# Kernel tuning notes

Hardware: AMD Instinct MI355X
Metric: run time of the kernel (lower is better)

## Reference

```python
import jax, jax.numpy as jnp
import numpy as np

B, A, C, H, W = 16, 5, 512, 16, 16


def _affine_grid(theta, Hh, Ww):
    # torch F.affine_grid, align_corners=False (default). theta: [2,3]
    xs = (2.0 * jnp.arange(Ww, dtype=jnp.float32) + 1.0) / Ww - 1.0  # [W]
    ys = (2.0 * jnp.arange(Hh, dtype=jnp.float32) + 1.0) / Hh - 1.0  # [H]
    gx = theta[0, 0] * xs[None, :] + theta[0, 1] * ys[:, None] + theta[0, 2]  # [H,W]
    gy = theta[1, 0] * xs[None, :] + theta[1, 1] * ys[:, None] + theta[1, 2]  # [H,W]
    return gx, gy


def _grid_sample(img, gx, gy):
    # torch F.grid_sample, bilinear, padding_mode='zeros', align_corners=False
    # img: [C,H,W]; gx,gy: [H,W] normalized coords
    C_, Hh, Ww = img.shape
    ix = ((gx + 1.0) * Ww - 1.0) * 0.5
    iy = ((gy + 1.0) * Hh - 1.0) * 0.5
    x0 = jnp.floor(ix); y0 = jnp.floor(iy)
    x1 = x0 + 1.0;      y1 = y0 + 1.0
    wx1 = ix - x0; wx0 = 1.0 - wx1
    wy1 = iy - y0; wy0 = 1.0 - wy1

    def gather(xi, yi):
        inb = (xi >= 0) & (xi < Ww) & (yi >= 0) & (yi < Hh)
        xc = jnp.clip(xi, 0, Ww - 1).astype(jnp.int32)
        yc = jnp.clip(yi, 0, Hh - 1).astype(jnp.int32)
        return img[:, yc, xc] * inb[None].astype(img.dtype)  # [C,H,W]

    return (gather(x0, y0) * (wx0 * wy0)[None] + gather(x1, y0) * (wx1 * wy0)[None]
          + gather(x0, y1) * (wx0 * wy1)[None] + gather(x1, y1) * (wx1 * wy1)[None])


def _warp(nb_feat, nb_warp):
    # nb_feat: [C,H,W] neighbor feature; nb_warp: [4,4] pose matrix
    zero = jnp.zeros((), dtype=jnp.float32)
    one = jnp.ones((), dtype=jnp.float32)
    theta_rot = jnp.stack([
        jnp.stack([nb_warp[0, 0], nb_warp[0, 1], zero]),
        jnp.stack([nb_warp[1, 0], nb_warp[1, 1], zero])])  # [2,3]
    gx_r, gy_r = _affine_grid(theta_rot, H, W)
    feat_rot = _grid_sample(nb_feat, gx_r, gy_r)
    x_trans = 4.0 * nb_warp[0, 3] / 128.0
    y_trans = -(4.0 * nb_warp[1, 3]) / 128.0
    theta_trans = jnp.stack([
        jnp.stack([one, zero, x_trans]),
        jnp.stack([zero, one, y_trans])])
    gx_t, gy_t = _affine_grid(theta_trans, H, W)
    return _grid_sample(feat_rot, gx_t, gy_t)  # [C,H,W]


def _fuse_one(local_b, trans_b, n):
    # local_b: [A,C,H,W], trans_b: [A,A,4,4], n: scalar num_agent
    # pair[i,j] = warp of agent j's feature into agent i's frame
    pair = jax.vmap(lambda t_i: jax.vmap(_warp)(local_b, t_i))(trans_b)  # [A,A,C,H,W]
    idx = jnp.arange(A)
    mask = (idx[:, None] != idx[None, :]) & (idx[:, None] < n) & (idx[None, :] < n)
    return local_b + jnp.einsum('ij,ijchw->ichw', mask.astype(local_b.dtype), pair)


def setup_inputs() -> dict:
    key = jax.random.key(0)
    k1, k2, k3, k4 = jax.random.split(key, 4)
    feat_maps = jax.random.normal(k1, (A * B, C, H, W), dtype=jnp.float32)
    # realistic near-rigid pose matrices: rotation block + translation column
    ang = jax.random.uniform(k2, (B, A, A), minval=-0.5, maxval=0.5)
    tr = jax.random.normal(k3, (B, A, A, 2), dtype=jnp.float32) * 8.0
    tm = jnp.zeros((B, A, A, 4, 4), dtype=jnp.float32)
    tm = tm.at[..., 0, 0].set(jnp.cos(ang)).at[..., 0, 1].set(-jnp.sin(ang))
    tm = tm.at[..., 1, 0].set(jnp.sin(ang)).at[..., 1, 1].set(jnp.cos(ang))
    tm = tm.at[..., 0, 3].set(tr[..., 0]).at[..., 1, 3].set(tr[..., 1])
    tm = tm.at[..., 2, 2].set(1.0).at[..., 3, 3].set(1.0)
    num_agent = jax.random.randint(k4, (B, A), 1, 6, dtype=jnp.int64) if jax.config.jax_enable_x64 else jax.random.randint(k4, (B, A), 1, 6, dtype=jnp.int32)
    return {"feat_maps": feat_maps, "trans_matrices": tm, "num_agent_tensor": num_agent}


def reference(feat_maps, trans_matrices, num_agent_tensor):
    # feat_maps is agent-major blocks of size B (feat_maps[B*i:B*(i+1)] is agent i)
    local = feat_maps.reshape(A, B, C, H, W).transpose(1, 0, 2, 3, 4)  # [B,A,C,H,W]
    fused = jax.vmap(_fuse_one)(local, trans_matrices, num_agent_tensor[:, 0])
    # agents2batch: concat agents along batch dim -> [A*B,C,H,W]
    return fused.transpose(1, 0, 2, 3, 4).reshape(A * B, C, H, W)
```

## Files before the change

kernel.cpp:

```cpp
#include <hip/hip_runtime.h>

#define NB 16
#define NA 5
#define NC 512
#define HW 256

typedef float f4 __attribute__((ext_vector_type(4)));

__global__ __launch_bounds__(256) void fafmimo_fuse_kernel(
    const float* __restrict__ feat,
    const float* __restrict__ trans,
    const int*   __restrict__ numa,
    float*       __restrict__ out)
{
    __shared__ f4 lds_src[NA][HW];
    __shared__ f4 lds_fr[HW];

    const int bx = blockIdx.x;
    const int b  = bx & (NB - 1);
    const int g  = bx >> 4;
    const int c0 = g << 2;
    const int p  = threadIdx.x;
    const int x  = p & 15, y = p >> 4;
    const float fx = (float)x - 7.5f;
    const float fy = (float)y - 7.5f;
    const int n = numa[b * NA];

    f4 local_v[NA];
#pragma unroll
    for (int a = 0; a < NA; ++a) {
        const float* src = feat + ((a * NB + b) * NC + c0) * HW + p;
        f4 v;
        v.x = src[0];
        v.y = src[HW];
        v.z = src[2 * HW];
        v.w = src[3 * HW];
        lds_src[a][p] = v;
        local_v[a] = v;
    }
    __syncthreads();

    for (int i = 0; i < NA; ++i) {
        f4 acc = local_v[i];

        if (i < n) {
            for (int j = 0; j < n; ++j) {
                if (j == i) continue;

                const f4* twv = (const f4*)(trans + (((b * NA) + i) * NA + j) * 16);
                const f4 row0 = twv[0];
                const f4 row1 = twv[1];

                const float ixr = row0.x * fx + row0.y * fy + 7.5f;
                const float iyr = row1.x * fx + row1.y * fy + 7.5f;
                const float fx0 = floorf(ixr), fy0 = floorf(iyr);
                const float wx1 = ixr - fx0, wx0 = 1.0f - wx1;
                const float wy1 = iyr - fy0, wy0 = 1.0f - wy1;
                const int ix0 = (int)fx0, iy0 = (int)fy0;
                const int ix1 = ix0 + 1,  iy1 = iy0 + 1;
                const float mx0 = (ix0 >= 0 && ix0 < 16) ? wx0 : 0.0f;
                const float mx1 = (ix1 >= 0 && ix1 < 16) ? wx1 : 0.0f;
                const float my0 = (iy0 >= 0 && iy0 < 16) ? wy0 : 0.0f;
                const float my1 = (iy1 >= 0 && iy1 < 16) ? wy1 : 0.0f;
                const int cx0 = min(max(ix0, 0), 15), cx1 = min(max(ix1, 0), 15);
                const int cy0 = min(max(iy0, 0), 15), cy1 = min(max(iy1, 0), 15);
                const f4 v00 = lds_src[j][cy0 * 16 + cx0];
                const f4 v01 = lds_src[j][cy0 * 16 + cx1];
                const f4 v10 = lds_src[j][cy1 * 16 + cx0];
                const f4 v11 = lds_src[j][cy1 * 16 + cx1];
                const f4 fr = (v00 * mx0 + v01 * mx1) * my0
                            + (v10 * mx0 + v11 * mx1) * my1;

                __syncthreads();
                lds_fr[p] = fr;
                __syncthreads();

                const float dx = 0.25f * row0.w;
                const float dy = -0.25f * row1.w;
                const float fdx = floorf(dx), fdy = floorf(dy);
                const float tx1 = dx - fdx, tx0 = 1.0f - tx1;
                const float ty1 = dy - fdy, ty0 = 1.0f - ty1;
                const int ox = x + (int)fdx;
                const int oy = y + (int)fdy;
                const float wxa = (ox     >= 0 && ox     < 16) ? tx0 : 0.0f;
                const float wxb = (ox + 1 >= 0 && ox + 1 < 16) ? tx1 : 0.0f;
                const float wya = (oy     >= 0 && oy     < 16) ? ty0 : 0.0f;
                const float wyb = (oy + 1 >= 0 && oy + 1 < 16) ? ty1 : 0.0f;
                const int cxa = min(max(ox, 0), 15),     cxb = min(max(ox + 1, 0), 15);
                const int cya = min(max(oy, 0), 15),     cyb = min(max(oy + 1, 0), 15);
                const f4 t00 = lds_fr[cya * 16 + cxa];
                const f4 t01 = lds_fr[cya * 16 + cxb];
                const f4 t10 = lds_fr[cyb * 16 + cxa];
                const f4 t11 = lds_fr[cyb * 16 + cxb];
                acc += (t00 * wxa + t01 * wxb) * wya
                     + (t10 * wxa + t11 * wxb) * wyb;
            }
        }

        float* dst = out + ((i * NB + b) * NC + c0) * HW + p;
        dst[0]      = acc.x;
        dst[HW]     = acc.y;
        dst[2 * HW] = acc.z;
        dst[3 * HW] = acc.w;
    }
}

extern "C" void kernel_launch(void* const* d_in, const int* in_sizes, int n_in,
                              void* d_out, int out_size, void* d_ws, size_t ws_size,
                              hipStream_t stream) {
    const float* feat  = (const float*)d_in[0];
    const float* trans = (const float*)d_in[1];
    const int*   numa  = (const int*)d_in[2];
    float* out = (float*)d_out;

    fafmimo_fuse_kernel<<<dim3(NB * (NC / 4)), dim3(256), 0, stream>>>(
        feat, trans, numa, out);
}
```

Before: 115.8 us.

## Store features as fp16 in LDS, fuse two-stage warp without syncs

Features are stored in LDS as packed fp16 with 8 channels per thread instead of 4 fp32, which halves the block count and doubles per-block channel work. The two-stage rotate-then-translate sampling is merged: each output pixel directly evaluates the four rotated samples its translation bilinear tap needs. That removes the intermediate LDS buffer and the two __syncthreads per neighbour. The cost is four times more rotation-sample work per neighbour, plus fp16 rounding of the inputs and of the interpolation arithmetic. That rounding may break accuracy tolerance, and the local feature is also rounded through fp16.

```diff
diff --git a/kernel.cpp b/kernel.cpp
--- a/kernel.cpp
+++ b/kernel.cpp
@@ -6,6 +6,33 @@
 #define HW 256
 
 typedef float f4 __attribute__((ext_vector_type(4)));
+typedef _Float16 h8 __attribute__((ext_vector_type(8)));
+
+static __device__ __forceinline__ h8 splat8(_Float16 v) {
+    h8 r = {v, v, v, v, v, v, v, v};
+    return r;
+}
+
+static __device__ __forceinline__ h8 rot_sample(const h8* __restrict__ src,
+                                                float ixr, float iyr, float ws) {
+    const float fx0 = floorf(ixr), fy0 = floorf(iyr);
+    const float wx1 = ixr - fx0,   wy1 = iyr - fy0;
+    const int ix0 = (int)fx0, iy0 = (int)fy0;
+    const int ix1 = ix0 + 1,  iy1 = iy0 + 1;
+    const float mx0 = (ix0 >= 0 && ix0 < 16) ? (1.0f - wx1) : 0.0f;
+    const float mx1 = (ix1 >= 0 && ix1 < 16) ? wx1 : 0.0f;
+    const float my0 = (iy0 >= 0 && iy0 < 16) ? (1.0f - wy1) * ws : 0.0f;
+    const float my1 = (iy1 >= 0 && iy1 < 16) ? wy1 * ws : 0.0f;
+    const int cx0 = min(max(ix0, 0), 15), cx1 = min(max(ix1, 0), 15);
+    const int cy0 = min(max(iy0, 0), 15), cy1 = min(max(iy1, 0), 15);
+    const h8 v00 = src[cy0 * 16 + cx0];
+    const h8 v01 = src[cy0 * 16 + cx1];
+    const h8 v10 = src[cy1 * 16 + cx0];
+    const h8 v11 = src[cy1 * 16 + cx1];
+    const h8 hx0 = splat8((_Float16)mx0), hx1 = splat8((_Float16)mx1);
+    const h8 hy0 = splat8((_Float16)my0), hy1 = splat8((_Float16)my1);
+    return (v00 * hx0 + v01 * hx1) * hy0 + (v10 * hx0 + v11 * hx1) * hy1;
+}
 
 __global__ __launch_bounds__(256) void fafmimo_fuse_kernel(
     const float* __restrict__ feat,
@@ -13,67 +40,41 @@
     const int*   __restrict__ numa,
     float*       __restrict__ out)
 {
-    __shared__ f4 lds_src[NA][HW];
-    __shared__ f4 lds_fr[HW];
+    __shared__ h8 lds_src[NA][HW];
 
     const int bx = blockIdx.x;
     const int b  = bx & (NB - 1);
     const int g  = bx >> 4;
-    const int c0 = g << 2;
+    const int c0 = g << 3;
     const int p  = threadIdx.x;
     const int x  = p & 15, y = p >> 4;
-    const float fx = (float)x - 7.5f;
-    const float fy = (float)y - 7.5f;
-    const int n = numa[b * NA];
+    const int n  = numa[b * NA];
 
-    f4 local_v[NA];
 #pragma unroll
     for (int a = 0; a < NA; ++a) {
         const float* src = feat + ((a * NB + b) * NC + c0) * HW + p;
-        f4 v;
-        v.x = src[0];
-        v.y = src[HW];
-        v.z = src[2 * HW];
-        v.w = src[3 * HW];
+        h8 v;
+#pragma unroll
+        for (int k = 0; k < 8; ++k) v[k] = (_Float16)src[k * HW];
         lds_src[a][p] = v;
-        local_v[a] = v;
     }
     __syncthreads();
 
     for (int i = 0; i < NA; ++i) {
-        f4 acc = local_v[i];
+        const h8 lv = lds_src[i][p];
+        float acc[8];
+#pragma unroll
+        for (int k = 0; k < 8; ++k) acc[k] = (float)lv[k];
 
         if (i < n) {
             for (int j = 0; j < n; ++j) {
                 if (j == i) continue;
 
-                const f4* twv = (const f4*)(trans + (((b * NA) + i) * NA + j) * 16);
-                const f4 row0 = twv[0];
-                const f4 row1 = twv[1];
-
-                const float ixr = row0.x * fx + row0.y * fy + 7.5f;
-                const float iyr = row1.x * fx + row1.y * fy + 7.5f;
-                const float fx0 = floorf(ixr), fy0 = floorf(iyr);
-                const float wx1 = ixr - fx0, wx0 = 1.0f - wx1;
-                const float wy1 = iyr - fy0, wy0 = 1.0f - wy1;
-                const int ix0 = (int)fx0, iy0 = (int)fy0;
-                const int ix1 = ix0 + 1,  iy1 = iy0 + 1;
-                const float mx0 = (ix0 >= 0 && ix0 < 16) ? wx0 : 0.0f;
-                const float mx1 = (ix1 >= 0 && ix1 < 16) ? wx1 : 0.0f;
-                const float my0 = (iy0 >= 0 && iy0 < 16) ? wy0 : 0.0f;
-                const float my1 = (iy1 >= 0 && iy1 < 16) ? wy1 : 0.0f;
-                const int cx0 = min(max(ix0, 0), 15), cx1 = min(max(ix1, 0), 15);
-                const int cy0 = min(max(iy0, 0), 15), cy1 = min(max(iy1, 0), 15);
-                const f4 v00 = lds_src[j][cy0 * 16 + cx0];
-                const f4 v01 = lds_src[j][cy0 * 16 + cx1];
-                const f4 v10 = lds_src[j][cy1 * 16 + cx0];
-                const f4 v11 = lds_src[j][cy1 * 16 + cx1];
-                const f4 fr = (v00 * mx0 + v01 * mx1) * my0
-                            + (v10 * mx0 + v11 * mx1) * my1;
-
-                __syncthreads();
-                lds_fr[p] = fr;
-                __syncthreads();
+                const f4* tw = (const f4*)(trans + (((b * NA) + i) * NA + j) * 16);
+                const f4 row0 = tw[0];
+                const f4 row1 = tw[1];
+                const float r00 = row0.x, r01 = row0.y;
+                const float r10 = row1.x, r11 = row1.y;
 
                 const float dx = 0.25f * row0.w;
                 const float dy = -0.25f * row1.w;
@@ -82,26 +83,34 @@
                 const float ty1 = dy - fdy, ty0 = 1.0f - ty1;
                 const int ox = x + (int)fdx;
                 const int oy = y + (int)fdy;
-                const float wxa = (ox     >= 0 && ox     < 16) ? tx0 : 0.0f;
-                const float wxb = (ox + 1 >= 0 && ox + 1 < 16) ? tx1 : 0.0f;
-                const float wya = (oy     >= 0 && oy     < 16) ? ty0 : 0.0f;
-                const float wyb = (oy + 1 >= 0 && oy + 1 < 16) ? ty1 : 0.0f;
-                const int cxa = min(max(ox, 0), 15),     cxb = min(max(ox + 1, 0), 15);
-                const int cya = min(max(oy, 0), 15),     cyb = min(max(oy + 1, 0), 15);
-                const f4 t00 = lds_fr[cya * 16 + cxa];
-                const f4 t01 = lds_fr[cya * 16 + cxb];
-                const f4 t10 = lds_fr[cyb * 16 + cxa];
-                const f4 t11 = lds_fr[cyb * 16 + cxb];
-                acc += (t00 * wxa + t01 * wxb) * wya
-                     + (t10 * wxa + t11 * wxb) * wyb;
+                const bool inx0 = (ox >= 0) && (ox < 16);
+                const bool inx1 = (ox + 1 >= 0) && (ox + 1 < 16);
+                const bool iny0 = (oy >= 0) && (oy < 16);
+                const bool iny1 = (oy + 1 >= 0) && (oy + 1 < 16);
+                const float ws00 = (inx0 && iny0) ? tx0 * ty0 : 0.0f;
+                const float ws10 = (inx1 && iny0) ? tx1 * ty0 : 0.0f;
+                const float ws01 = (inx0 && iny1) ? tx0 * ty1 : 0.0f;
+                const float ws11 = (inx1 && iny1) ? tx1 * ty1 : 0.0f;
+
+                const float fox = (float)ox - 7.5f;
+                const float foy = (float)oy - 7.5f;
+                const float bxr = r00 * fox + r01 * foy + 7.5f;
+                const float byr = r10 * fox + r11 * foy + 7.5f;
+
+                const h8* srcj = &lds_src[j][0];
+                h8 pacc = rot_sample(srcj, bxr,             byr,             ws00);
+                pacc   += rot_sample(srcj, bxr + r00,       byr + r10,       ws10);
+                pacc   += rot_sample(srcj, bxr + r01,       byr + r11,       ws01);
+                pacc   += rot_sample(srcj, bxr + r00 + r01, byr + r10 + r11, ws11);
+
+#pragma unroll
+                for (int k = 0; k < 8; ++k) acc[k] += (float)pacc[k];
             }
         }
 
         float* dst = out + ((i * NB + b) * NC + c0) * HW + p;
-        dst[0]      = acc.x;
-        dst[HW]     = acc.y;
-        dst[2 * HW] = acc.z;
-        dst[3 * HW] = acc.w;
+#pragma unroll
+        for (int k = 0; k < 8; ++k) dst[k * HW] = acc[k];
     }
 }
 
@@ -113,6 +122,6 @@
     const int*   numa  = (const int*)d_in[2];
     float* out = (float*)d_out;
 
-    fafmimo_fuse_kernel<<<dim3(NB * (NC / 4)), dim3(256), 0, stream>>>(
+    fafmimo_fuse_kernel<<<dim3(NB * (NC / 8)), dim3(256), 0, stream>>>(
         feat, trans, numa, out);
 }
```

Result: slower. 142.6 us (+23.1%).
